# Kernel tuning notes

Hardware: AMD Instinct MI355X
Metric: run time of the kernel (lower is better)

Reference implementation:

```python
import jax, jax.numpy as jnp
import numpy as np

N_NODES = 10000
N_EDGES = 160000
HIDDEN = 256
HEADS = 8
LN_EPS = 1e-5


def setup_inputs() -> dict:
    key = jax.random.key(0)
    ks = jax.random.split(key, 8)
    s = 1.0 / np.sqrt(HIDDEN)
    return {
        "node_embeddings": jax.random.normal(ks[0], (1, N_NODES, HIDDEN), jnp.float32),
        "edge_index": jax.random.randint(ks[1], (2, N_EDGES), 0, N_NODES, dtype=jnp.int32),
        "Wq": jax.random.normal(ks[2], (HIDDEN, HIDDEN), jnp.float32) * s,
        "Wk": jax.random.normal(ks[3], (HIDDEN, HIDDEN), jnp.float32) * s,
        "Wv": jax.random.normal(ks[4], (HIDDEN, HIDDEN), jnp.float32) * s,
        "Wo": jax.random.normal(ks[5], (HIDDEN, HIDDEN), jnp.float32) * s,
        "ln_gamma": jnp.ones((HIDDEN,), jnp.float32),
        "ln_beta": jnp.zeros((HIDDEN,), jnp.float32),
    }


def reference(node_embeddings, edge_index, Wq, Wk, Wv, Wo, ln_gamma, ln_beta):
    B, N, Dm = node_embeddings.shape
    H = HEADS
    hd = Dm // H
    scale = 1.0 / np.sqrt(hd)

    def heads(x):  # [B,N,Dm] -> [B,H,N,hd]
        return x.reshape(B, N, H, hd).transpose(0, 2, 1, 3)

    Q = heads(node_embeddings @ Wq)
    K = heads(node_embeddings @ Wk)
    V = heads(node_embeddings @ Wv)

    src, dst = edge_index[0], edge_index[1]
    Qe = Q[:, :, src, :]           # [B,H,E,hd]
    Ke = K[:, :, dst, :]
    Ve = V[:, :, dst, :]

    scores = jnp.einsum('bhed,bhed->bhe', Qe, Ke) * scale   # [B,H,E]
    s_t = scores.transpose(2, 0, 1)                          # [E,B,H]
    smax = jax.ops.segment_max(s_t, src, num_segments=N)    # [N,B,H]
    ex = jnp.exp(s_t - smax[src])                            # [E,B,H]
    denom = jax.ops.segment_sum(ex, src, num_segments=N)    # [N,B,H]
    attn = ex / denom[src]                                   # scatter-softmax weights

    wV = attn[..., None] * Ve.transpose(2, 0, 1, 3)          # [E,B,H,hd]
    agg = jax.ops.segment_sum(wV, src, num_segments=N)      # [N,B,H,hd]
    attn_out = agg.transpose(1, 0, 2, 3).reshape(B, N, Dm)   # [B,N,Dm]

    out = attn_out @ Wo
    x = out + node_embeddings
    mu = jnp.mean(x, axis=-1, keepdims=True)
    var = jnp.mean((x - mu) ** 2, axis=-1, keepdims=True)
    return (x - mu) * jax.lax.rsqrt(var + LN_EPS) * ln_gamma + ln_beta
```

## Files before the change

### kernel.cpp

```cpp
#include <hip/hip_runtime.h>

#define NN 10000
#define NE 160000
#define DM 256
#define CAP 96
#define LN_EPSF 1e-5f
#define SCALEF 0.17677669529663687f

typedef unsigned short u16;
typedef __attribute__((ext_vector_type(4))) u16 u16x4;
typedef __attribute__((ext_vector_type(8))) u16 u16x8;
typedef __attribute__((ext_vector_type(4))) float f32x4;
typedef __attribute__((ext_vector_type(8))) short short8;

__device__ __forceinline__ float b2f(u16 u) { return __uint_as_float(((unsigned)u) << 16); }
__device__ __forceinline__ u16 f2b(float f) {
    unsigned u = __float_as_uint(f);
    return (u16)((u + 0x7fffu + ((u >> 16) & 1u)) >> 16);
}
__device__ __forceinline__ int clampi(int v) { return v < 0 ? 0 : (v >= NN ? NN - 1 : v); }

__global__ void k_fill_zero_f32(float* __restrict__ o, int n) {
    int i = blockIdx.x * 256 + threadIdx.x;
    if (i < n) o[i] = 0.f;
}

#define UPD(mm, ss, AA, kv, p) do {                  \
    float nm_ = fmaxf(mm, p);                        \
    float al_ = __expf(mm - nm_);                    \
    float pe_ = __expf(p - nm_);                     \
    ss = ss * al_ + pe_;                             \
    AA[0] = AA[0] * al_ + pe_ * b2f(kv[4]);          \
    AA[1] = AA[1] * al_ + pe_ * b2f(kv[5]);          \
    AA[2] = AA[2] * al_ + pe_ * b2f(kv[6]);          \
    AA[3] = AA[3] * al_ + pe_ * b2f(kv[7]);          \
    mm = nm_;                                        \
} while (0)

__global__ void k_prep(const float* __restrict__ Wq, const float* __restrict__ Wk,
                       const float* __restrict__ Wv, const float* __restrict__ Wo,
                       u16* __restrict__ Wt, int* __restrict__ cnt) {
    int id = blockIdx.x * 256 + threadIdx.x;
    if (id < NN) cnt[id] = 0;
    int m = id >> 16;
    int rc = id & 65535;
    int r = rc >> 8, c = rc & 255;
    const float* W = (m == 0) ? Wq : (m == 1) ? Wk : (m == 2) ? Wv : Wo;
    Wt[m * 65536 + c * 256 + r] = f2b(W[r * 256 + c]);
}

__global__ __launch_bounds__(256) void k_qkv_bucket(const float* __restrict__ X, const u16* __restrict__ Wt,
                                                    u16* __restrict__ Q, u16* __restrict__ KV,
                                                    const int* __restrict__ EI, int* __restrict__ cnt,
                                                    int* __restrict__ buck) {
    constexpr int BS = 40;
    constexpr int ASF = 264;
    __shared__ u16 At[64 * ASF];
    __shared__ u16 Bt[256 * BS];
    if (blockIdx.y == 1) {
        int e = blockIdx.x * 256 + threadIdx.x;
        if (e < NE) {
            int s = clampi(EI[e]);
            int slot = atomicAdd(&cnt[s], 1);
            if (slot < CAP) buck[s * CAP + slot] = clampi(EI[NE + e]);
        }
        return;
    }
    if (blockIdx.x >= 157) return;
    const int t = threadIdx.x;
    const int w = t >> 6, l = t & 63, quad = l >> 4, m16 = l & 15;
    const int node0 = blockIdx.x * 64;
    const int arow = t >> 2, ac8 = (t & 3) * 8;
    const int anode = node0 + arow;
#pragma unroll
    for (int k0 = 0; k0 < DM; k0 += 32) {
        u16x8 av = {0, 0, 0, 0, 0, 0, 0, 0};
        if (anode < NN) {
            const float* xp = X + (size_t)anode * DM + k0 + ac8;
            f32x4 a0 = *(const f32x4*)(xp);
            f32x4 a1 = *(const f32x4*)(xp + 4);
            av[0] = f2b(a0[0]); av[1] = f2b(a0[1]); av[2] = f2b(a0[2]); av[3] = f2b(a0[3]);
            av[4] = f2b(a1[0]); av[5] = f2b(a1[1]); av[6] = f2b(a1[2]); av[7] = f2b(a1[3]);
        }
        *(u16x8*)(At + arow * ASF + k0 + ac8) = av;
    }
    __syncthreads();
    for (int mat = 0; mat < 3; mat++) {
        const u16* Wm = Wt + mat * 65536;
        f32x4 acc[4][4];
#pragma unroll
        for (int i = 0; i < 4; i++)
#pragma unroll
            for (int j = 0; j < 4; j++) acc[i][j] = (f32x4){0.f, 0.f, 0.f, 0.f};
        for (int k0 = 0; k0 < DM; k0 += 32) {
            const u16* bsrc = Wm + t * DM + k0;
            u16x8 b0 = *(const u16x8*)(bsrc);
            u16x8 b1 = *(const u16x8*)(bsrc + 8);
            u16x8 b2 = *(const u16x8*)(bsrc + 16);
            u16x8 b3 = *(const u16x8*)(bsrc + 24);
            u16* bd = Bt + t * BS;
            *(u16x8*)(bd) = b0;
            *(u16x8*)(bd + 8) = b1;
            *(u16x8*)(bd + 16) = b2;
            *(u16x8*)(bd + 24) = b3;
            __syncthreads();
            short8 a[4], b[4];
#pragma unroll
            for (int rt = 0; rt < 4; rt++)
                a[rt] = *(const short8*)(At + (rt * 16 + m16) * ASF + k0 + quad * 8);
#pragma unroll
            for (int ct = 0; ct < 4; ct++)
                b[ct] = *(const short8*)(Bt + (w * 64 + ct * 16 + m16) * BS + quad * 8);
#pragma unroll
            for (int rt = 0; rt < 4; rt++)
#pragma unroll
                for (int ct = 0; ct < 4; ct++)
                    acc[rt][ct] = __builtin_amdgcn_mfma_f32_16x16x32_bf16(a[rt], b[ct], acc[rt][ct], 0, 0, 0);
            __syncthreads();
        }
#pragma unroll
        for (int rt = 0; rt < 4; rt++) {
#pragma unroll
            for (int ct = 0; ct < 4; ct++) {
                int col = w * 64 + ct * 16 + m16;
#pragma unroll
                for (int r = 0; r < 4; r++) {
                    int node = node0 + rt * 16 + quad * 4 + r;
                    if (node < NN) {
                        u16 v = f2b(acc[rt][ct][r]);
                        if (mat == 0) Q[(size_t)node * DM + col] = v;
                        else KV[(size_t)node * 512 + (col >> 2) * 8 + (col & 3) + ((mat == 2) ? 4 : 0)] = v;
                    }
                }
            }
        }
    }
}

__global__ __launch_bounds__(256) void k_edge(const u16* __restrict__ Q, const u16* __restrict__ KV,
                                              const int* __restrict__ cnt, const int* __restrict__ buck,
                                              u16* __restrict__ attn) {
    const int t = threadIdx.x;
    const int w = t >> 6, l = t & 63;
    const int node = blockIdx.x * 4 + w;
    const int d0 = l * 4;
    int deg = cnt[node];
    if (deg > CAP) deg = CAP;
    const int* bl = buck + node * CAP;
    u16x4 q4 = *(const u16x4*)(Q + (size_t)node * DM + d0);
    float qf0 = b2f(q4[0]) * SCALEF, qf1 = b2f(q4[1]) * SCALEF;
    float qf2 = b2f(q4[2]) * SCALEF, qf3 = b2f(q4[3]) * SCALEF;
    float mm[8], ss[8];
    f32x4 AA[8];
#pragma unroll
    for (int j = 0; j < 8; j++) {
        mm[j] = -3.0e38f;
        ss[j] = 0.f;
        AA[j] = (f32x4){0.f, 0.f, 0.f, 0.f};
    }
    int i = 0;
    int deg8 = deg & ~7;
    for (; i < deg8; i += 8) {
        int4 ea = *(const int4*)(bl + i);
        int4 eb = *(const int4*)(bl + i + 4);
        int dst[8] = {ea.x, ea.y, ea.z, ea.w, eb.x, eb.y, eb.z, eb.w};
        u16x8 kv[8];
#pragma unroll
        for (int j = 0; j < 8; j++)
            kv[j] = *(const u16x8*)(KV + (size_t)dst[j] * 512 + l * 8);
        float p[8];
#pragma unroll
        for (int j = 0; j < 8; j++)
            p[j] = qf0 * b2f(kv[j][0]) + qf1 * b2f(kv[j][1]) + qf2 * b2f(kv[j][2]) + qf3 * b2f(kv[j][3]);
#pragma unroll
        for (int j = 0; j < 8; j++) p[j] += __shfl_xor(p[j], 1, 64);
#pragma unroll
        for (int j = 0; j < 8; j++) p[j] += __shfl_xor(p[j], 2, 64);
#pragma unroll
        for (int j = 0; j < 8; j++) p[j] += __shfl_xor(p[j], 4, 64);
#pragma unroll
        for (int j = 0; j < 8; j++) UPD(mm[j], ss[j], AA[j], kv[j], p[j]);
    }
    for (; i < deg; ++i) {
        int dst = bl[i];
        u16x8 kv = *(const u16x8*)(KV + (size_t)dst * 512 + l * 8);
        float p = qf0 * b2f(kv[0]) + qf1 * b2f(kv[1]) + qf2 * b2f(kv[2]) + qf3 * b2f(kv[3]);
        p += __shfl_xor(p, 1, 64);
        p += __shfl_xor(p, 2, 64);
        p += __shfl_xor(p, 4, 64);
        UPD(mm[0], ss[0], AA[0], kv, p);
    }
    float nm = mm[0];
#pragma unroll
    for (int j = 1; j < 8; j++) nm = fmaxf(nm, mm[j]);
    float S = 0.f, O0 = 0.f, O1 = 0.f, O2 = 0.f, O3 = 0.f;
#pragma unroll
    for (int j = 0; j < 8; j++) {
        float wj = __expf(mm[j] - nm);
        S += ss[j] * wj;
        O0 += AA[j][0] * wj;
        O1 += AA[j][1] * wj;
        O2 += AA[j][2] * wj;
        O3 += AA[j][3] * wj;
    }
    float inv = (S > 0.f) ? 1.f / S : 0.f;
    u16x4 o;
    o[0] = f2b(O0 * inv);
    o[1] = f2b(O1 * inv);
    o[2] = f2b(O2 * inv);
    o[3] = f2b(O3 * inv);
    *(u16x4*)(attn + (size_t)node * DM + d0) = o;
}

__global__ __launch_bounds__(256) void k_gemm_out_ln(const u16* __restrict__ In, const u16* __restrict__ WoT,
                                                     const float* __restrict__ X, const float* __restrict__ g,
                                                     const float* __restrict__ b, float* __restrict__ out) {
    constexpr int BS = 40;
    constexpr int ALS = 264;
    __shared__ u16 AtL[32 * ALS];
    __shared__ u16 Bt[256 * BS];
    __shared__ float gbuf[256], bbuf[256];
    __shared__ float redS[4][32], redQ[4][32], muS[32], rsS[32];
    const int t = threadIdx.x;
    gbuf[t] = g[t];
    bbuf[t] = b[t];
    const int w = t >> 6, l = t & 63, quad = l >> 4, m16 = l & 15;
    const int node0 = blockIdx.x * 32;
    {
        const int arow = t >> 3, ac32 = (t & 7) * 32;
        const int anode = node0 + arow;
#pragma unroll
        for (int j = 0; j < 4; j++) {
            u16x8 av = {0, 0, 0, 0, 0, 0, 0, 0};
            if (anode < NN) av = *(const u16x8*)(In + (size_t)anode * DM + ac32 + j * 8);
            *(u16x8*)(AtL + arow * ALS + ac32 + j * 8) = av;
        }
    }
    f32x4 acc[2][4];
#pragma unroll
    for (int i = 0; i < 2; i++)
#pragma unroll
        for (int j = 0; j < 4; j++) acc[i][j] = (f32x4){0.f, 0.f, 0.f, 0.f};
    __syncthreads();
    for (int k0 = 0; k0 < DM; k0 += 32) {
        const u16* bsrc = WoT + t * DM + k0;
        u16x8 b0 = *(const u16x8*)(bsrc);
        u16x8 b1 = *(const u16x8*)(bsrc + 8);
        u16x8 b2 = *(const u16x8*)(bsrc + 16);
        u16x8 b3 = *(const u16x8*)(bsrc + 24);
        u16* bd = Bt + t * BS;
        *(u16x8*)(bd) = b0;
        *(u16x8*)(bd + 8) = b1;
        *(u16x8*)(bd + 16) = b2;
        *(u16x8*)(bd + 24) = b3;
        __syncthreads();
        short8 a[2], bf[4];
#pragma unroll
        for (int rt = 0; rt < 2; rt++)
            a[rt] = *(const short8*)(AtL + (rt * 16 + m16) * ALS + k0 + quad * 8);
#pragma unroll
        for (int ct = 0; ct < 4; ct++)
            bf[ct] = *(const short8*)(Bt + (w * 64 + ct * 16 + m16) * BS + quad * 8);
#pragma unroll
        for (int rt = 0; rt < 2; rt++)
#pragma unroll
            for (int ct = 0; ct < 4; ct++)
                acc[rt][ct] = __builtin_amdgcn_mfma_f32_16x16x32_bf16(a[rt], bf[ct], acc[rt][ct], 0, 0, 0);
        __syncthreads();
    }
#pragma unroll
    for (int rt = 0; rt < 2; rt++)
#pragma unroll
        for (int ct = 0; ct < 4; ct++) {
            int col = w * 64 + ct * 16 + m16;
#pragma unroll
            for (int r = 0; r < 4; r++) {
                int node = node0 + rt * 16 + quad * 4 + r;
                float x = (node < NN) ? X[(size_t)node * DM + col] : 0.f;
                acc[rt][ct][r] += x;
            }
        }
#pragma unroll
    for (int rt = 0; rt < 2; rt++) {
#pragma unroll
        for (int r = 0; r < 4; r++) {
            float p1 = acc[rt][0][r] + acc[rt][1][r] + acc[rt][2][r] + acc[rt][3][r];
            float p2 = acc[rt][0][r] * acc[rt][0][r] + acc[rt][1][r] * acc[rt][1][r] +
                       acc[rt][2][r] * acc[rt][2][r] + acc[rt][3][r] * acc[rt][3][r];
#pragma unroll
            for (int o = 1; o < 16; o <<= 1) {
                p1 += __shfl_xor(p1, o, 64);
                p2 += __shfl_xor(p2, o, 64);
            }
            if (m16 == 0) {
                int row = rt * 16 + quad * 4 + r;
                redS[w][row] = p1;
                redQ[w][row] = p2;
            }
        }
    }
    __syncthreads();
    if (t < 32) {
        float s1t = redS[0][t] + redS[1][t] + redS[2][t] + redS[3][t];
        float s2t = redQ[0][t] + redQ[1][t] + redQ[2][t] + redQ[3][t];
        float mm = s1t * (1.f / DM);
        float var = s2t * (1.f / DM) - mm * mm;
        muS[t] = mm;
        rsS[t] = rsqrtf(var + LN_EPSF);
    }
    __syncthreads();
#pragma unroll
    for (int rt = 0; rt < 2; rt++)
#pragma unroll
        for (int ct = 0; ct < 4; ct++) {
            int col = w * 64 + ct * 16 + m16;
#pragma unroll
            for (int r = 0; r < 4; r++) {
                int row = rt * 16 + quad * 4 + r;
                int node = node0 + row;
                if (node < NN)
                    out[(size_t)node * DM + col] = (acc[rt][ct][r] - muS[row]) * rsS[row] * gbuf[col] + bbuf[col];
            }
        }
}

extern "C" void kernel_launch(void* const* d_in, const int* in_sizes, int n_in,
                              void* d_out, int out_size, void* d_ws, size_t ws_size,
                              hipStream_t stream) {
    (void)in_sizes; (void)n_in;
    const float* X  = (const float*)d_in[0];
    const int*   EI = (const int*)d_in[1];
    const float* Wq = (const float*)d_in[2];
    const float* Wk = (const float*)d_in[3];
    const float* Wv = (const float*)d_in[4];
    const float* Wo = (const float*)d_in[5];
    const float* g  = (const float*)d_in[6];
    const float* be = (const float*)d_in[7];

    const size_t SWT  = (size_t)4 * 65536 * 2;
    const size_t SKV  = (size_t)NN * 512 * 2;
    const size_t SCNT = (size_t)NN * 4;
    const size_t SBK  = (size_t)NN * CAP * 4;
    const size_t SQB  = (size_t)NN * DM * 2;
    const size_t SAT  = (size_t)NN * DM * 2;
    const size_t need = SWT + SKV + SCNT + SBK + SQB + SAT;
    if (ws_size < need) {
        k_fill_zero_f32<<<(out_size + 255) / 256, 256, 0, stream>>>((float*)d_out, out_size);
        return;
    }
    char* p = (char*)d_ws;
    u16* Wt   = (u16*)p; p += SWT;
    u16* KVb  = (u16*)p; p += SKV;
    int* cnt  = (int*)p; p += SCNT;
    int* buck = (int*)p; p += SBK;
    u16* Qb   = (u16*)p; p += SQB;
    u16* attn = (u16*)p; p += SAT;

    k_prep<<<1024, 256, 0, stream>>>(Wq, Wk, Wv, Wo, Wt, cnt);
    k_qkv_bucket<<<dim3(625, 2), 256, 0, stream>>>(X, Wt, Qb, KVb, EI, cnt, buck);
    k_edge<<<NN / 4, 256, 0, stream>>>(Qb, KVb, cnt, buck, attn);
    k_gemm_out_ln<<<313, 256, 0, stream>>>(attn, Wt + 3 * 65536, X, g, be, (float*)d_out);
}
```

Baseline: 152.7 us.

## Split QKV GEMM per matrix across grid and read weights directly from global

The QKV projection kernel now launches one block per 32-node tile per matrix (grid y selects Q, K or V) instead of one 64-node block looping over all three matrices. This exposes about three times as many GEMM blocks. The bucketing blocks now handle two edges per thread. Both GEMM kernels drop the LDS staging of weight tiles and the per-k-step barriers, loading B fragments straight from global memory (L2-resident weights), which trades shared-memory traffic and syncs for more global loads and re-converting X once per matrix.

```diff
diff --git a/kernel.cpp b/kernel.cpp
--- a/kernel.cpp
+++ b/kernel.cpp
@@ -53,84 +53,74 @@
                                                     u16* __restrict__ Q, u16* __restrict__ KV,
                                                     const int* __restrict__ EI, int* __restrict__ cnt,
                                                     int* __restrict__ buck) {
-    constexpr int BS = 40;
-    constexpr int ASF = 264;
-    __shared__ u16 At[64 * ASF];
-    __shared__ u16 Bt[256 * BS];
-    if (blockIdx.y == 1) {
-        int e = blockIdx.x * 256 + threadIdx.x;
-        if (e < NE) {
-            int s = clampi(EI[e]);
-            int slot = atomicAdd(&cnt[s], 1);
-            if (slot < CAP) buck[s * CAP + slot] = clampi(EI[NE + e]);
+    constexpr int ALS = 264;
+    __shared__ u16 AtL[32 * ALS];
+    if (blockIdx.y == 3) {
+        int e0 = blockIdx.x * 512 + threadIdx.x;
+#pragma unroll
+        for (int h = 0; h < 2; h++) {
+            int e = e0 + h * 256;
+            if (e < NE) {
+                int s = clampi(EI[e]);
+                int slot = atomicAdd(&cnt[s], 1);
+                if (slot < CAP) buck[s * CAP + slot] = clampi(EI[NE + e]);
+            }
         }
         return;
     }
-    if (blockIdx.x >= 157) return;
     const int t = threadIdx.x;
     const int w = t >> 6, l = t & 63, quad = l >> 4, m16 = l & 15;
-    const int node0 = blockIdx.x * 64;
-    const int arow = t >> 2, ac8 = (t & 3) * 8;
-    const int anode = node0 + arow;
-#pragma unroll
+    const int mat = blockIdx.y;
+    const u16* Wm = Wt + mat * 65536;
+    const int node0 = blockIdx.x * 32;
+    {
+        const int arow = t >> 3, ac32 = (t & 7) * 32;
+        const int anode = node0 + arow;
+#pragma unroll
+        for (int j = 0; j < 4; j++) {
+            u16x8 av = {0, 0, 0, 0, 0, 0, 0, 0};
+            if (anode < NN) {
+                const float* xp = X + (size_t)anode * DM + ac32 + j * 8;
+                f32x4 a0 = *(const f32x4*)(xp);
+                f32x4 a1 = *(const f32x4*)(xp + 4);
+                av[0] = f2b(a0[0]); av[1] = f2b(a0[1]); av[2] = f2b(a0[2]); av[3] = f2b(a0[3]);
+                av[4] = f2b(a1[0]); av[5] = f2b(a1[1]); av[6] = f2b(a1[2]); av[7] = f2b(a1[3]);
+            }
+            *(u16x8*)(AtL + arow * ALS + ac32 + j * 8) = av;
+        }
+    }
+    __syncthreads();
+    f32x4 acc[2][4];
+#pragma unroll
+    for (int i = 0; i < 2; i++)
+#pragma unroll
+        for (int j = 0; j < 4; j++) acc[i][j] = (f32x4){0.f, 0.f, 0.f, 0.f};
     for (int k0 = 0; k0 < DM; k0 += 32) {
-        u16x8 av = {0, 0, 0, 0, 0, 0, 0, 0};
-        if (anode < NN) {
-            const float* xp = X + (size_t)anode * DM + k0 + ac8;
-            f32x4 a0 = *(const f32x4*)(xp);
-            f32x4 a1 = *(const f32x4*)(xp + 4);
-            av[0] = f2b(a0[0]); av[1] = f2b(a0[1]); av[2] = f2b(a0[2]); av[3] = f2b(a0[3]);
-            av[4] = f2b(a1[0]); av[5] = f2b(a1[1]); av[6] = f2b(a1[2]); av[7] = f2b(a1[3]);
-        }
-        *(u16x8*)(At + arow * ASF + k0 + ac8) = av;
-    }
-    __syncthreads();
-    for (int mat = 0; mat < 3; mat++) {
-        const u16* Wm = Wt + mat * 65536;
-        f32x4 acc[4][4];
-#pragma unroll
-        for (int i = 0; i < 4; i++)
-#pragma unroll
-            for (int j = 0; j < 4; j++) acc[i][j] = (f32x4){0.f, 0.f, 0.f, 0.f};
-        for (int k0 = 0; k0 < DM; k0 += 32) {
-            const u16* bsrc = Wm + t * DM + k0;
-            u16x8 b0 = *(const u16x8*)(bsrc);
-            u16x8 b1 = *(const u16x8*)(bsrc + 8);
-            u16x8 b2 = *(const u16x8*)(bsrc + 16);
-            u16x8 b3 = *(const u16x8*)(bsrc + 24);
-            u16* bd = Bt + t * BS;
-            *(u16x8*)(bd) = b0;
-            *(u16x8*)(bd + 8) = b1;
-            *(u16x8*)(bd + 16) = b2;
-            *(u16x8*)(bd + 24) = b3;
-            __syncthreads();
-            short8 a[4], b[4];
-#pragma unroll
-            for (int rt = 0; rt < 4; rt++)
-                a[rt] = *(const short8*)(At + (rt * 16 + m16) * ASF + k0 + quad * 8);
+        short8 a[2], b[4];
+#pragma unroll
+        for (int rt = 0; rt < 2; rt++)
+            a[rt] = *(const short8*)(AtL + (rt * 16 + m16) * ALS + k0 + quad * 8);
+#pragma unroll
+        for (int ct = 0; ct < 4; ct++)
+            b[ct] = *(const short8*)(Wm + (size_t)(w * 64 + ct * 16 + m16) * DM + k0 + quad * 8);
+#pragma unroll
+        for (int rt = 0; rt < 2; rt++)
 #pragma unroll
             for (int ct = 0; ct < 4; ct++)
-                b[ct] = *(const short8*)(Bt + (w * 64 + ct * 16 + m16) * BS + quad * 8);
-#pragma unroll
-            for (int rt = 0; rt < 4; rt++)
-#pragma unroll
-                for (int ct = 0; ct < 4; ct++)
-                    acc[rt][ct] = __builtin_amdgcn_mfma_f32_16x16x32_bf16(a[rt], b[ct], acc[rt][ct], 0, 0, 0);
-            __syncthreads();
-        }
-#pragma unroll
-        for (int rt = 0; rt < 4; rt++) {
-#pragma unroll
-            for (int ct = 0; ct < 4; ct++) {
-                int col = w * 64 + ct * 16 + m16;
-#pragma unroll
-                for (int r = 0; r < 4; r++) {
-                    int node = node0 + rt * 16 + quad * 4 + r;
-                    if (node < NN) {
-                        u16 v = f2b(acc[rt][ct][r]);
-                        if (mat == 0) Q[(size_t)node * DM + col] = v;
-                        else KV[(size_t)node * 512 + (col >> 2) * 8 + (col & 3) + ((mat == 2) ? 4 : 0)] = v;
-                    }
+                acc[rt][ct] = __builtin_amdgcn_mfma_f32_16x16x32_bf16(a[rt], b[ct], acc[rt][ct], 0, 0, 0);
+    }
+#pragma unroll
+    for (int rt = 0; rt < 2; rt++) {
+#pragma unroll
+        for (int ct = 0; ct < 4; ct++) {
+            int col = w * 64 + ct * 16 + m16;
+#pragma unroll
+            for (int r = 0; r < 4; r++) {
+                int node = node0 + rt * 16 + quad * 4 + r;
+                if (node < NN) {
+                    u16 v = f2b(acc[rt][ct][r]);
+                    if (mat == 0) Q[(size_t)node * DM + col] = v;
+                    else KV[(size_t)node * 512 + (col >> 2) * 8 + (col & 3) + ((mat == 2) ? 4 : 0)] = v;
                 }
             }
         }
@@ -215,10 +205,8 @@
 __global__ __launch_bounds__(256) void k_gemm_out_ln(const u16* __restrict__ In, const u16* __restrict__ WoT,
                                                      const float* __restrict__ X, const float* __restrict__ g,
                                                      const float* __restrict__ b, float* __restrict__ out) {
-    constexpr int BS = 40;
     constexpr int ALS = 264;
     __shared__ u16 AtL[32 * ALS];
-    __shared__ u16 Bt[256 * BS];
     __shared__ float gbuf[256], bbuf[256];
     __shared__ float redS[4][32], redQ[4][32], muS[32], rsS[32];
     const int t = threadIdx.x;
@@ -236,37 +224,25 @@
             *(u16x8*)(AtL + arow * ALS + ac32 + j * 8) = av;
         }
     }
+    __syncthreads();
     f32x4 acc[2][4];
 #pragma unroll
     for (int i = 0; i < 2; i++)
 #pragma unroll
         for (int j = 0; j < 4; j++) acc[i][j] = (f32x4){0.f, 0.f, 0.f, 0.f};
-    __syncthreads();
     for (int k0 = 0; k0 < DM; k0 += 32) {
-        const u16* bsrc = WoT + t * DM + k0;
-        u16x8 b0 = *(const u16x8*)(bsrc);
-        u16x8 b1 = *(const u16x8*)(bsrc + 8);
-        u16x8 b2 = *(const u16x8*)(bsrc + 16);
-        u16x8 b3 = *(const u16x8*)(bsrc + 24);
-        u16* bd = Bt + t * BS;
-        *(u16x8*)(bd) = b0;
-        *(u16x8*)(bd + 8) = b1;
-        *(u16x8*)(bd + 16) = b2;
-        *(u16x8*)(bd + 24) = b3;
-        __syncthreads();
         short8 a[2], bf[4];
 #pragma unroll
         for (int rt = 0; rt < 2; rt++)
             a[rt] = *(const short8*)(AtL + (rt * 16 + m16) * ALS + k0 + quad * 8);
 #pragma unroll
         for (int ct = 0; ct < 4; ct++)
-            bf[ct] = *(const short8*)(Bt + (w * 64 + ct * 16 + m16) * BS + quad * 8);
+            bf[ct] = *(const short8*)(WoT + (size_t)(w * 64 + ct * 16 + m16) * DM + k0 + quad * 8);
 #pragma unroll
         for (int rt = 0; rt < 2; rt++)
 #pragma unroll
             for (int ct = 0; ct < 4; ct++)
                 acc[rt][ct] = __builtin_amdgcn_mfma_f32_16x16x32_bf16(a[rt], bf[ct], acc[rt][ct], 0, 0, 0);
-        __syncthreads();
     }
 #pragma unroll
     for (int rt = 0; rt < 2; rt++)
@@ -357,7 +333,7 @@
     u16* attn = (u16*)p; p += SAT;
 
     k_prep<<<1024, 256, 0, stream>>>(Wq, Wk, Wv, Wo, Wt, cnt);
-    k_qkv_bucket<<<dim3(625, 2), 256, 0, stream>>>(X, Wt, Qb, KVb, EI, cnt, buck);
+    k_qkv_bucket<<<dim3(313, 4), 256, 0, stream>>>(X, Wt, Qb, KVb, EI, cnt, buck);
     k_edge<<<NN / 4, 256, 0, stream>>>(Qb, KVb, cnt, buck, attn);
     k_gemm_out_ln<<<313, 256, 0, stream>>>(attn, Wt + 3 * 65536, X, g, be, (float*)d_out);
 }
```

Result: no change. 150.9 us (-1.2%).
